# Performance work log

Measured on AMD Instinct MI355X. Metric: run time of the kernel, lower is better.

Reference implementation:

```python
import jax, jax.numpy as jnp
import numpy as np

EPS = 1e-5

def conv1d(x, w, b):
    # x: (N,C,L), w: (O,I,3), stride 1, padding 1 -> same length
    y = jax.lax.conv_general_dilated(x, w, window_strides=(1,), padding=((1, 1),),
                                     dimension_numbers=('NCH', 'OIH', 'NCH'))
    return y + b[None, :, None]

def bn(x, g, b):
    # BatchNorm1d, training-mode batch statistics over (N, L) per channel
    m = x.mean(axis=(0, 2), keepdims=True)
    v = x.var(axis=(0, 2), keepdims=True)
    return (x - m) * jax.lax.rsqrt(v + EPS) * g[None, :, None] + b[None, :, None]

def setup_inputs() -> dict:
    V, E, H, L, NL = 50257, 512, 512, 2048, 2
    D = 1 + NL * 2  # 5 channels in the pre-attention conv stack
    key = jax.random.key(0)
    ks = iter(jax.random.split(key, 48))
    def rn(shape, s=0.02):
        return jax.random.normal(next(ks), shape, dtype=jnp.float32) * s
    inp = dict(
        emb=rn((V, E), 1.0),
        conv1_w=rn((32, D, 3)), conv1_b=rn((32,)),
        conv2_w=rn((D, 32, 3)), conv2_b=rn((D,)),
        conv3_w=rn((1, D, 3)), conv3_b=rn((1,)),
        conv4_w=rn((32, 3, 3)), conv4_b=rn((32,)),
        conv5_w=rn((3, 32, 3)), conv5_b=rn((3,)),
        conv6_w=rn((1, 3, 3)), conv6_b=rn((1,)),
        bn1_g=jnp.ones((32,)), bn1_b=jnp.zeros((32,)),
        bn2_g=jnp.ones((D,)), bn2_b=jnp.zeros((D,)),
        bn3_g=jnp.ones((1,)), bn3_b=jnp.zeros((1,)),
        bn4_g=jnp.ones((32,)), bn4_b=jnp.zeros((32,)),
        bn5_g=jnp.ones((3,)), bn5_b=jnp.zeros((3,)),
        bn6_g=jnp.ones((1,)), bn6_b=jnp.zeros((1,)),
        att_w=rn((L, E)), att_b=rn((L,)),
        gru_wih=rn((4, 3 * H, E)), gru_whh=rn((4, 3 * H, H)),
        gru_bih=rn((4, 3 * H)), gru_bhh=rn((4, 3 * H)),
        lo_w=rn((V, H)), lo_b=rn((V,)),
        h_state=rn((4, 1, H), 1.0),
        encoder_outs=rn((L, 2 * H), 1.0),
        x=jax.random.randint(next(ks), (1,), 0, V),
    )
    return inp

def reference(emb, conv1_w, conv1_b, conv2_w, conv2_b, conv3_w, conv3_b,
              conv4_w, conv4_b, conv5_w, conv5_b, conv6_w, conv6_b,
              bn1_g, bn1_b, bn2_g, bn2_b, bn3_g, bn3_b,
              bn4_g, bn4_b, bn5_g, bn5_b, bn6_g, bn6_b,
              att_w, att_b, gru_wih, gru_whh, gru_bih, gru_bhh,
              lo_w, lo_b, h_state, encoder_outs, x):
    H = h_state.shape[-1]
    # dropout(p=0.1) treated as identity (eval mode / deterministic reference)
    embadded = emb[x].reshape(1, 1, H)                                      # (1,1,512)
    pre = jnp.concatenate([h_state.reshape(1, -1, H), embadded], axis=1)    # (1,5,512)
    c = jax.nn.relu(bn(conv1d(pre, conv1_w, conv1_b), bn1_g, bn1_b))        # (1,32,512)
    pre = jax.nn.relu(bn(conv1d(c, conv2_w, conv2_b) + pre, bn2_g, bn2_b))  # residual, (1,5,512)
    pre = jax.nn.relu(bn(conv1d(pre, conv3_w, conv3_b), bn3_g, bn3_b))      # (1,1,512)
    aw = jax.nn.softmax(pre.reshape(1, -1) @ att_w.T + att_b, axis=1)       # (1,L)
    app = (aw @ encoder_outs).reshape(1, -1, H)                             # (1,2,512) (bidir encoder)
    com = jnp.concatenate([app, embadded], axis=1)                          # (1,3,512)
    c = jax.nn.relu(bn(conv1d(com, conv4_w, conv4_b), bn4_g, bn4_b))        # (1,32,512)
    com = jax.nn.relu(bn(conv1d(c, conv5_w, conv5_b) + com, bn5_g, bn5_b))  # residual, (1,3,512)
    com = jax.nn.relu(bn(conv1d(com, conv6_w, conv6_b), bn6_g, bn6_b))      # (1,1,512)
    # 4-layer stacked GRU, single time step, batch 1 (PyTorch gate order r,z,n)
    xt = com.reshape(H)
    h_new = []
    for l in range(h_state.shape[0]):
        gi = gru_wih[l] @ xt + gru_bih[l]
        gh = gru_whh[l] @ h_state[l, 0] + gru_bhh[l]
        ir, iz, inn = jnp.split(gi, 3)
        hr, hz, hn = jnp.split(gh, 3)
        r = jax.nn.sigmoid(ir + hr)
        z = jax.nn.sigmoid(iz + hz)
        n = jnp.tanh(inn + r * hn)
        xt = (1.0 - z) * n + z * h_state[l, 0]
        h_new.append(xt)
    h_state_new = jnp.stack(h_new)[:, None, :]                              # (4,1,512)
    out = jax.nn.log_softmax((xt @ lo_w.T + lo_b)[None, :], axis=1)         # (1,V)
    return out, h_state_new
```

## Files before the change

### kernel.cpp

```cpp
#include <hip/hip_runtime.h>
#include <hip/hip_bf16.h>

typedef __attribute__((ext_vector_type(4))) float f32x4;

constexpr int WSF_Q     = 0;
constexpr int WSF_ADEN  = 512;
constexpr int WSF_APART = 1024;
constexpr int WSF_XT    = 33792;
constexpr int WSF_LOGV  = 36352;
constexpr int WSF_PM    = 86624;
constexpr int WSF_PS    = 87424;
constexpr int NVOCAB    = 50257;
constexpr int NBLK_V    = 786;

__device__ __forceinline__ float wave_rsum(float v) {
#pragma unroll
    for (int o = 32; o > 0; o >>= 1) v += __shfl_down(v, o);
    return v;
}
__device__ __forceinline__ float sigm(float x) { return 1.0f / (1.0f + __expf(-x)); }

__global__ __launch_bounds__(512) void k_pre(
    const float* __restrict__ emb, const int* __restrict__ xidx,
    const float* __restrict__ hstate,
    const float* __restrict__ w1, const float* __restrict__ b1,
    const float* __restrict__ w2, const float* __restrict__ b2,
    const float* __restrict__ w3, const float* __restrict__ b3,
    const float* __restrict__ g1, const float* __restrict__ bb1,
    const float* __restrict__ g2, const float* __restrict__ bb2,
    const float* __restrict__ g3, const float* __restrict__ bb3,
    float* __restrict__ ws)
{
    constexpr int W1 = 0, B1 = 480, G1 = 512, BB1 = 544;
    constexpr int W2 = 576, B2 = 1056, G2 = 1061, BB2 = 1066;
    constexpr int W3 = 1071, B3 = 1086, G3 = 1087, BB3 = 1088, NW = 1089;
    __shared__ float s_w[NW];
    __shared__ float s_pre[5][512];
    __shared__ float s_y[32][512];
    __shared__ float s_stat[32][2];
    const int tid = threadIdx.x, lane = tid & 63, wid = tid >> 6, l = tid;

    if (tid < 480) s_w[W1 + tid] = w1[tid];
    if (tid < 32) { s_w[B1 + tid] = b1[tid]; s_w[G1 + tid] = g1[tid]; s_w[BB1 + tid] = bb1[tid]; }
    if (tid < 480) s_w[W2 + tid] = w2[tid];
    if (tid < 5) { s_w[B2 + tid] = b2[tid]; s_w[G2 + tid] = g2[tid]; s_w[BB2 + tid] = bb2[tid]; }
    if (tid < 15) s_w[W3 + tid] = w3[tid];
    if (tid == 0) { s_w[B3] = b3[0]; s_w[G3] = g3[0]; s_w[BB3] = bb3[0]; }

    const int x = xidx[0];
#pragma unroll
    for (int c = 0; c < 4; ++c) s_pre[c][l] = hstate[c * 512 + l];
    s_pre[4][l] = emb[(size_t)x * 512 + l];
    __syncthreads();

    float px[5][3];
#pragma unroll
    for (int ic = 0; ic < 5; ++ic) {
        px[ic][0] = (l > 0)   ? s_pre[ic][l-1] : 0.f;
        px[ic][1] =             s_pre[ic][l];
        px[ic][2] = (l < 511) ? s_pre[ic][l+1] : 0.f;
    }
#pragma unroll 4
    for (int oc = 0; oc < 32; ++oc) {
        float a = s_w[B1 + oc];
#pragma unroll
        for (int ic = 0; ic < 5; ++ic)
#pragma unroll
            for (int k = 0; k < 3; ++k)
                a += s_w[W1 + oc*15 + ic*3 + k] * px[ic][k];
        s_y[oc][l] = a;
    }
    __syncthreads();
#pragma unroll
    for (int t = 0; t < 4; ++t) {
        const int oc = wid * 4 + t;
        float s = 0.f, s2 = 0.f;
#pragma unroll
        for (int j = 0; j < 8; ++j) { float v = s_y[oc][lane + j*64]; s += v; s2 += v*v; }
        s = wave_rsum(s); s2 = wave_rsum(s2);
        if (lane == 0) { float m = s/512.f, var = s2/512.f - m*m; s_stat[oc][0] = m; s_stat[oc][1] = rsqrtf(var + 1e-5f); }
    }
    __syncthreads();
#pragma unroll 4
    for (int oc = 0; oc < 32; ++oc)
        s_y[oc][l] = fmaxf((s_y[oc][l] - s_stat[oc][0]) * s_stat[oc][1] * s_w[G1+oc] + s_w[BB1+oc], 0.f);
    __syncthreads();

    float y2[5];
#pragma unroll
    for (int oc = 0; oc < 5; ++oc) y2[oc] = s_w[B2 + oc];
#pragma unroll 2
    for (int ic = 0; ic < 32; ++ic) {
        float c0 = (l > 0)   ? s_y[ic][l-1] : 0.f;
        float c1 =             s_y[ic][l];
        float c2 = (l < 511) ? s_y[ic][l+1] : 0.f;
#pragma unroll
        for (int oc = 0; oc < 5; ++oc) {
            const int base = W2 + (oc*32 + ic)*3;
            y2[oc] += s_w[base]*c0 + s_w[base+1]*c1 + s_w[base+2]*c2;
        }
    }
#pragma unroll
    for (int oc = 0; oc < 5; ++oc) y2[oc] += s_pre[oc][l];
    __syncthreads();
#pragma unroll
    for (int oc = 0; oc < 5; ++oc) s_y[oc][l] = y2[oc];
    __syncthreads();
    if (wid < 5) {
        const int oc = wid;
        float s = 0.f, s2 = 0.f;
#pragma unroll
        for (int j = 0; j < 8; ++j) { float v = s_y[oc][lane + j*64]; s += v; s2 += v*v; }
        s = wave_rsum(s); s2 = wave_rsum(s2);
        if (lane == 0) { float m = s/512.f, var = s2/512.f - m*m; s_stat[oc][0] = m; s_stat[oc][1] = rsqrtf(var + 1e-5f); }
    }
    __syncthreads();
#pragma unroll
    for (int oc = 0; oc < 5; ++oc)
        s_pre[oc][l] = fmaxf((y2[oc] - s_stat[oc][0]) * s_stat[oc][1] * s_w[G2+oc] + s_w[BB2+oc], 0.f);
    __syncthreads();

    float a3 = s_w[B3];
#pragma unroll
    for (int ic = 0; ic < 5; ++ic) {
        float c0 = (l > 0)   ? s_pre[ic][l-1] : 0.f;
        float c1 =             s_pre[ic][l];
        float c2 = (l < 511) ? s_pre[ic][l+1] : 0.f;
        a3 += s_w[W3+ic*3]*c0 + s_w[W3+ic*3+1]*c1 + s_w[W3+ic*3+2]*c2;
    }
    s_y[0][l] = a3;
    __syncthreads();
    if (wid == 0) {
        float s = 0.f, s2 = 0.f;
#pragma unroll
        for (int j = 0; j < 8; ++j) { float v = s_y[0][lane + j*64]; s += v; s2 += v*v; }
        s = wave_rsum(s); s2 = wave_rsum(s2);
        if (lane == 0) { float m = s/512.f, var = s2/512.f - m*m; s_stat[0][0] = m; s_stat[0][1] = rsqrtf(var + 1e-5f); }
    }
    __syncthreads();
    ws[WSF_Q + l] = fmaxf((a3 - s_stat[0][0]) * s_stat[0][1] * s_w[G3] + s_w[BB3], 0.f);
}

__global__ __launch_bounds__(256) void k_att(
    const float* __restrict__ attw, const float* __restrict__ attb,
    const float* __restrict__ enc, float* __restrict__ ws)
{
    __shared__ float s_e[64];
    __shared__ float s_d[4];
    const int tid = threadIdx.x, lane = tid & 63, wid = tid >> 6;
    const int jc = blockIdx.x;

    float q0[4], q1[4];
#pragma unroll
    for (int j = 0; j < 4; ++j) {
        q0[j] = ws[WSF_Q + lane*4 + j];
        q1[j] = ws[WSF_Q + 256 + lane*4 + j];
    }
    float dpart = 0.f;
#pragma unroll 4
    for (int r = 0; r < 16; ++r) {
        const int row = jc * 64 + wid * 16 + r;
        f32x4 w0 = *(const f32x4*)(attw + (size_t)row*512 + lane*4);
        f32x4 w1 = *(const f32x4*)(attw + (size_t)row*512 + 256 + lane*4);
        float a = 0.f;
#pragma unroll
        for (int j = 0; j < 4; ++j) a += w0[j]*q0[j] + w1[j]*q1[j];
        a = wave_rsum(a);
        if (lane == 0) {
            float e = __expf(a + attb[row]);
            s_e[wid*16 + r] = e;
            dpart += e;
        }
    }
    if (lane == 0) s_d[wid] = dpart;
    __syncthreads();
    if (tid == 0) ws[WSF_ADEN + jc] = s_d[0] + s_d[1] + s_d[2] + s_d[3];

    const int col = tid * 4;
    const float* ep = enc + (size_t)(jc * 64) * 1024 + col;
    f32x4 acc = {0.f, 0.f, 0.f, 0.f};
#pragma unroll 8
    for (int jj = 0; jj < 64; ++jj) {
        f32x4 v = *(const f32x4*)(ep + (size_t)jj * 1024);
        acc += s_e[jj] * v;
    }
    *(f32x4*)(ws + WSF_APART + jc * 1024 + col) = acc;
}

__global__ __launch_bounds__(512) void k_post(
    const float* __restrict__ emb, const int* __restrict__ xidx,
    const float* __restrict__ w4, const float* __restrict__ b4,
    const float* __restrict__ w5, const float* __restrict__ b5,
    const float* __restrict__ w6, const float* __restrict__ b6,
    const float* __restrict__ g4, const float* __restrict__ bb4,
    const float* __restrict__ g5, const float* __restrict__ bb5,
    const float* __restrict__ g6, const float* __restrict__ bb6,
    float* __restrict__ ws)
{
    constexpr int W4 = 0, B4 = 288, G4 = 320, BB4 = 352;
    constexpr int W5 = 384, B5 = 672, G5 = 675, BB5 = 678;
    constexpr int W6 = 681, B6 = 690, G6 = 691, BB6 = 692, NW = 693;
    __shared__ float s_w[NW];
    __shared__ float s_com[3][512];
    __shared__ float s_y[32][512];
    __shared__ float s_stat[32][2];
    const int tid = threadIdx.x, lane = tid & 63, wid = tid >> 6, l = tid;

    if (tid < 288) s_w[W4 + tid] = w4[tid];
    if (tid < 32) { s_w[B4 + tid] = b4[tid]; s_w[G4 + tid] = g4[tid]; s_w[BB4 + tid] = bb4[tid]; }
    if (tid < 288) s_w[W5 + tid] = w5[tid];
    if (tid < 3) { s_w[B5 + tid] = b5[tid]; s_w[G5 + tid] = g5[tid]; s_w[BB5 + tid] = bb5[tid]; }
    if (tid < 9) s_w[W6 + tid] = w6[tid];
    if (tid == 0) { s_w[B6] = b6[0]; s_w[G6] = g6[0]; s_w[BB6] = bb6[0]; }

    float den = 0.f;
#pragma unroll 8
    for (int i = 0; i < 32; ++i) den += ws[WSF_ADEN + i];
    const float invS = 1.0f / den;
    float a0 = 0.f, a1 = 0.f;
#pragma unroll 8
    for (int p = 0; p < 32; ++p) {
        a0 += ws[WSF_APART + p*1024 + l];
        a1 += ws[WSF_APART + p*1024 + 512 + l];
    }
    const int x = xidx[0];
    s_com[0][l] = a0 * invS;
    s_com[1][l] = a1 * invS;
    s_com[2][l] = emb[(size_t)x*512 + l];
    __syncthreads();

    float px[3][3];
#pragma unroll
    for (int ic = 0; ic < 3; ++ic) {
        px[ic][0] = (l > 0)   ? s_com[ic][l-1] : 0.f;
        px[ic][1] =             s_com[ic][l];
        px[ic][2] = (l < 511) ? s_com[ic][l+1] : 0.f;
    }
#pragma unroll 4
    for (int oc = 0; oc < 32; ++oc) {
        float a = s_w[B4 + oc];
#pragma unroll
        for (int ic = 0; ic < 3; ++ic)
#pragma unroll
            for (int k = 0; k < 3; ++k)
                a += s_w[W4 + oc*9 + ic*3 + k] * px[ic][k];
        s_y[oc][l] = a;
    }
    __syncthreads();
#pragma unroll
    for (int t = 0; t < 4; ++t) {
        const int oc = wid * 4 + t;
        float s = 0.f, s2 = 0.f;
#pragma unroll
        for (int j = 0; j < 8; ++j) { float v = s_y[oc][lane + j*64]; s += v; s2 += v*v; }
        s = wave_rsum(s); s2 = wave_rsum(s2);
        if (lane == 0) { float m = s/512.f, var = s2/512.f - m*m; s_stat[oc][0] = m; s_stat[oc][1] = rsqrtf(var + 1e-5f); }
    }
    __syncthreads();
#pragma unroll 4
    for (int oc = 0; oc < 32; ++oc)
        s_y[oc][l] = fmaxf((s_y[oc][l] - s_stat[oc][0]) * s_stat[oc][1] * s_w[G4+oc] + s_w[BB4+oc], 0.f);
    __syncthreads();

    float y2[3];
#pragma unroll
    for (int oc = 0; oc < 3; ++oc) y2[oc] = s_w[B5 + oc];
#pragma unroll 2
    for (int ic = 0; ic < 32; ++ic) {
        float c0 = (l > 0)   ? s_y[ic][l-1] : 0.f;
        float c1 =             s_y[ic][l];
        float c2 = (l < 511) ? s_y[ic][l+1] : 0.f;
#pragma unroll
        for (int oc = 0; oc < 3; ++oc) {
            const int base = W5 + (oc*32 + ic)*3;
            y2[oc] += s_w[base]*c0 + s_w[base+1]*c1 + s_w[base+2]*c2;
        }
    }
#pragma unroll
    for (int oc = 0; oc < 3; ++oc) y2[oc] += s_com[oc][l];
    __syncthreads();
#pragma unroll
    for (int oc = 0; oc < 3; ++oc) s_y[oc][l] = y2[oc];
    __syncthreads();
    if (wid < 3) {
        const int oc = wid;
        float s = 0.f, s2 = 0.f;
#pragma unroll
        for (int j = 0; j < 8; ++j) { float v = s_y[oc][lane + j*64]; s += v; s2 += v*v; }
        s = wave_rsum(s); s2 = wave_rsum(s2);
        if (lane == 0) { float m = s/512.f, var = s2/512.f - m*m; s_stat[oc][0] = m; s_stat[oc][1] = rsqrtf(var + 1e-5f); }
    }
    __syncthreads();
#pragma unroll
    for (int oc = 0; oc < 3; ++oc)
        s_com[oc][l] = fmaxf((y2[oc] - s_stat[oc][0]) * s_stat[oc][1] * s_w[G5+oc] + s_w[BB5+oc], 0.f);
    __syncthreads();

    float a6 = s_w[B6];
#pragma unroll
    for (int ic = 0; ic < 3; ++ic) {
        float c0 = (l > 0)   ? s_com[ic][l-1] : 0.f;
        float c1 =             s_com[ic][l];
        float c2 = (l < 511) ? s_com[ic][l+1] : 0.f;
        a6 += s_w[W6+ic*3]*c0 + s_w[W6+ic*3+1]*c1 + s_w[W6+ic*3+2]*c2;
    }
    s_y[0][l] = a6;
    __syncthreads();
    if (wid == 0) {
        float s = 0.f, s2 = 0.f;
#pragma unroll
        for (int j = 0; j < 8; ++j) { float v = s_y[0][lane + j*64]; s += v; s2 += v*v; }
        s = wave_rsum(s); s2 = wave_rsum(s2);
        if (lane == 0) { float m = s/512.f, var = s2/512.f - m*m; s_stat[0][0] = m; s_stat[0][1] = rsqrtf(var + 1e-5f); }
    }
    __syncthreads();
    ws[WSF_XT + l] = fmaxf((a6 - s_stat[0][0]) * s_stat[0][1] * s_w[G6] + s_w[BB6], 0.f);
}

__global__ __launch_bounds__(256) void k_gru(
    const float* __restrict__ wih, const float* __restrict__ whh,
    const float* __restrict__ bih, const float* __restrict__ bhh,
    const float* __restrict__ hstate,
    const float* __restrict__ xt_in, float* __restrict__ xt_out,
    float* __restrict__ hout, int layer)
{
    wih += (size_t)layer * 1536 * 512;
    whh += (size_t)layer * 1536 * 512;
    bih += layer * 1536;
    bhh += layer * 1536;
    const float* hp = hstate + layer * 512;

    const int tid = threadIdx.x, lane = tid & 63, wid = tid >> 6;
    float xq0[4], xq1[4], hq0[4], hq1[4];
#pragma unroll
    for (int j = 0; j < 4; ++j) {
        xq0[j] = xt_in[lane*4 + j];
        xq1[j] = xt_in[256 + lane*4 + j];
        hq0[j] = hp[lane*4 + j];
        hq1[j] = hp[256 + lane*4 + j];
    }
    __shared__ float s_g[8][6];
    const int i0 = blockIdx.x * 8;
#pragma unroll
    for (int t = 0; t < 2; ++t) {
        const int ii = wid * 2 + t;
        const int i = i0 + ii;
        float a[6] = {0.f, 0.f, 0.f, 0.f, 0.f, 0.f};
#pragma unroll
        for (int g = 0; g < 3; ++g) {
            const float* wr = wih + (size_t)(i + g*512) * 512;
            f32x4 w0 = *(const f32x4*)(wr + lane*4);
            f32x4 w1 = *(const f32x4*)(wr + 256 + lane*4);
#pragma unroll
            for (int j = 0; j < 4; ++j) a[g] += w0[j]*xq0[j] + w1[j]*xq1[j];
        }
#pragma unroll
        for (int g = 0; g < 3; ++g) {
            const float* wr = whh + (size_t)(i + g*512) * 512;
            f32x4 w0 = *(const f32x4*)(wr + lane*4);
            f32x4 w1 = *(const f32x4*)(wr + 256 + lane*4);
#pragma unroll
            for (int j = 0; j < 4; ++j) a[3+g] += w0[j]*hq0[j] + w1[j]*hq1[j];
        }
#pragma unroll
        for (int g = 0; g < 6; ++g) a[g] = wave_rsum(a[g]);
        if (lane == 0) {
#pragma unroll
            for (int g = 0; g < 6; ++g) s_g[ii][g] = a[g];
        }
    }
    __syncthreads();
    if (tid < 8) {
        const int i = i0 + tid;
        float ir = s_g[tid][0] + bih[i];
        float iz = s_g[tid][1] + bih[i + 512];
        float in_ = s_g[tid][2] + bih[i + 1024];
        float hr = s_g[tid][3] + bhh[i];
        float hz = s_g[tid][4] + bhh[i + 512];
        float hn = s_g[tid][5] + bhh[i + 1024];
        float r = sigm(ir + hr);
        float z = sigm(iz + hz);
        float n = tanhf(in_ + r * hn);
        float h = (1.f - z) * n + z * hp[i];
        xt_out[i] = h;
        hout[i] = h;
    }
}

__global__ __launch_bounds__(256) void k_vocab(
    const float* __restrict__ low, const float* __restrict__ lob,
    float* __restrict__ ws)
{
    const int tid = threadIdx.x, lane = tid & 63, wid = tid >> 6;
    float q0[4], q1[4];
#pragma unroll
    for (int j = 0; j < 4; ++j) {
        q0[j] = ws[WSF_XT + 4*512 + lane*4 + j];
        q1[j] = ws[WSF_XT + 4*512 + 256 + lane*4 + j];
    }
    const int row0 = blockIdx.x * 64 + wid * 16;
    float m = -INFINITY, s = 0.0f;
#pragma unroll 4
    for (int r = 0; r < 16; ++r) {
        const int row = row0 + r;
        if (row < NVOCAB) {
            f32x4 w0 = *(const f32x4*)(low + (size_t)row*512 + lane*4);
            f32x4 w1 = *(const f32x4*)(low + (size_t)row*512 + 256 + lane*4);
            float a = 0.f;
#pragma unroll
            for (int j = 0; j < 4; ++j) a += w0[j]*q0[j] + w1[j]*q1[j];
            a = wave_rsum(a);
            if (lane == 0) {
                float v = a + lob[row];
                ws[WSF_LOGV + row] = v;
                if (v > m) { s = s * __expf(m - v) + 1.0f; m = v; }
                else       { s += __expf(v - m); }
            }
        }
    }
    __shared__ float smx[4], ssx[4];
    if (lane == 0) { smx[wid] = m; ssx[wid] = s; }
    __syncthreads();
    if (tid == 0) {
        float M = -INFINITY, S = 0.0f;
#pragma unroll
        for (int w = 0; w < 4; ++w) {
            float mb = smx[w], sb = ssx[w];
            if (sb > 0.0f) {
                if (mb > M) { S = S * __expf(M - mb) + sb; M = mb; }
                else        { S += sb * __expf(mb - M); }
            }
        }
        ws[WSF_PM + blockIdx.x] = M;
        ws[WSF_PS + blockIdx.x] = S;
    }
}

__global__ __launch_bounds__(256) void k_outlse(
    const float* __restrict__ ws, float* __restrict__ out)
{
    __shared__ float smx[256], ssx[256];
    const int tid = threadIdx.x;
    float M = -INFINITY, S = 0.0f;
    for (int i = tid; i < NBLK_V; i += 256) {
        float mb = ws[WSF_PM + i], sb = ws[WSF_PS + i];
        if (mb > M) { S = S * __expf(M - mb) + sb; M = mb; }
        else        { S += sb * __expf(mb - M); }
    }
    smx[tid] = M; ssx[tid] = S;
    __syncthreads();
    for (int st = 128; st > 0; st >>= 1) {
        if (tid < st) {
            float mb = smx[tid + st], sb = ssx[tid + st];
            if (sb > 0.0f) {
                if (mb > smx[tid]) { ssx[tid] = ssx[tid] * __expf(smx[tid] - mb) + sb; smx[tid] = mb; }
                else               { ssx[tid] += sb * __expf(mb - smx[tid]); }
            }
        }
        __syncthreads();
    }
    const float lse = smx[0] + logf(ssx[0]);
    const int i = blockIdx.x * 256 + tid;
    if (i < NVOCAB) out[i] = ws[WSF_LOGV + i] - lse;
}

extern "C" void kernel_launch(void* const* d_in, const int* in_sizes, int n_in,
                              void* d_out, int out_size, void* d_ws, size_t ws_size,
                              hipStream_t stream)
{
    (void)in_sizes; (void)n_in; (void)out_size; (void)ws_size;
    const float* emb     = (const float*)d_in[0];
    const float* conv1_w = (const float*)d_in[1];  const float* conv1_b = (const float*)d_in[2];
    const float* conv2_w = (const float*)d_in[3];  const float* conv2_b = (const float*)d_in[4];
    const float* conv3_w = (const float*)d_in[5];  const float* conv3_b = (const float*)d_in[6];
    const float* conv4_w = (const float*)d_in[7];  const float* conv4_b = (const float*)d_in[8];
    const float* conv5_w = (const float*)d_in[9];  const float* conv5_b = (const float*)d_in[10];
    const float* conv6_w = (const float*)d_in[11]; const float* conv6_b = (const float*)d_in[12];
    const float* bn1_g = (const float*)d_in[13];   const float* bn1_b = (const float*)d_in[14];
    const float* bn2_g = (const float*)d_in[15];   const float* bn2_b = (const float*)d_in[16];
    const float* bn3_g = (const float*)d_in[17];   const float* bn3_b = (const float*)d_in[18];
    const float* bn4_g = (const float*)d_in[19];   const float* bn4_b = (const float*)d_in[20];
    const float* bn5_g = (const float*)d_in[21];   const float* bn5_b = (const float*)d_in[22];
    const float* bn6_g = (const float*)d_in[23];   const float* bn6_b = (const float*)d_in[24];
    const float* att_w = (const float*)d_in[25];   const float* att_b = (const float*)d_in[26];
    const float* gru_wih = (const float*)d_in[27]; const float* gru_whh = (const float*)d_in[28];
    const float* gru_bih = (const float*)d_in[29]; const float* gru_bhh = (const float*)d_in[30];
    const float* lo_w = (const float*)d_in[31];    const float* lo_b = (const float*)d_in[32];
    const float* h_state = (const float*)d_in[33];
    const float* enc = (const float*)d_in[34];
    const int* x = (const int*)d_in[35];

    float* ws = (float*)d_ws;
    float* out = (float*)d_out;

    k_pre<<<1, 512, 0, stream>>>(emb, x, h_state,
        conv1_w, conv1_b, conv2_w, conv2_b, conv3_w, conv3_b,
        bn1_g, bn1_b, bn2_g, bn2_b, bn3_g, bn3_b, ws);
    k_att<<<32, 256, 0, stream>>>(att_w, att_b, enc, ws);
    k_post<<<1, 512, 0, stream>>>(emb, x,
        conv4_w, conv4_b, conv5_w, conv5_b, conv6_w, conv6_b,
        bn4_g, bn4_b, bn5_g, bn5_b, bn6_g, bn6_b, ws);
    for (int l = 0; l < 4; ++l) {
        k_gru<<<64, 256, 0, stream>>>(gru_wih, gru_whh, gru_bih, gru_bhh, h_state,
            ws + WSF_XT + l * 512, ws + WSF_XT + (l + 1) * 512,
            out + NVOCAB + l * 512, l);
    }
    k_vocab<<<NBLK_V, 256, 0, stream>>>(lo_w, lo_b, ws);
    k_outlse<<<197, 256, 0, stream>>>(ws, out);
}
```

Baseline: 96.56 us.

## Spread attention and GRU matvecs across more blocks for higher parallelism

```diff
diff --git a/kernel.cpp b/kernel.cpp
--- a/kernel.cpp
+++ b/kernel.cpp
@@ -6,10 +6,10 @@
 constexpr int WSF_Q     = 0;
 constexpr int WSF_ADEN  = 512;
 constexpr int WSF_APART = 1024;
-constexpr int WSF_XT    = 33792;
-constexpr int WSF_LOGV  = 36352;
-constexpr int WSF_PM    = 86624;
-constexpr int WSF_PS    = 87424;
+constexpr int WSF_XT    = 132096;
+constexpr int WSF_LOGV  = 134656;
+constexpr int WSF_PM    = 184960;
+constexpr int WSF_PS    = 185856;
 constexpr int NVOCAB    = 50257;
 constexpr int NBLK_V    = 786;
 
@@ -145,7 +145,7 @@
     const float* __restrict__ attw, const float* __restrict__ attb,
     const float* __restrict__ enc, float* __restrict__ ws)
 {
-    __shared__ float s_e[64];
+    __shared__ float s_e[16];
     __shared__ float s_d[4];
     const int tid = threadIdx.x, lane = tid & 63, wid = tid >> 6;
     const int jc = blockIdx.x;
@@ -157,9 +157,9 @@
         q1[j] = ws[WSF_Q + 256 + lane*4 + j];
     }
     float dpart = 0.f;
-#pragma unroll 4
-    for (int r = 0; r < 16; ++r) {
-        const int row = jc * 64 + wid * 16 + r;
+#pragma unroll
+    for (int r = 0; r < 4; ++r) {
+        const int row = jc * 16 + wid * 4 + r;
         f32x4 w0 = *(const f32x4*)(attw + (size_t)row*512 + lane*4);
         f32x4 w1 = *(const f32x4*)(attw + (size_t)row*512 + 256 + lane*4);
         float a = 0.f;
@@ -168,7 +168,7 @@
         a = wave_rsum(a);
         if (lane == 0) {
             float e = __expf(a + attb[row]);
-            s_e[wid*16 + r] = e;
+            s_e[wid*4 + r] = e;
             dpart += e;
         }
     }
@@ -177,10 +177,10 @@
     if (tid == 0) ws[WSF_ADEN + jc] = s_d[0] + s_d[1] + s_d[2] + s_d[3];
 
     const int col = tid * 4;
-    const float* ep = enc + (size_t)(jc * 64) * 1024 + col;
+    const float* ep = enc + (size_t)(jc * 16) * 1024 + col;
     f32x4 acc = {0.f, 0.f, 0.f, 0.f};
 #pragma unroll 8
-    for (int jj = 0; jj < 64; ++jj) {
+    for (int jj = 0; jj < 16; ++jj) {
         f32x4 v = *(const f32x4*)(ep + (size_t)jj * 1024);
         acc += s_e[jj] * v;
     }
@@ -215,11 +215,11 @@
 
     float den = 0.f;
 #pragma unroll 8
-    for (int i = 0; i < 32; ++i) den += ws[WSF_ADEN + i];
+    for (int i = 0; i < 128; ++i) den += ws[WSF_ADEN + i];
     const float invS = 1.0f / den;
     float a0 = 0.f, a1 = 0.f;
 #pragma unroll 8
-    for (int p = 0; p < 32; ++p) {
+    for (int p = 0; p < 128; ++p) {
         a0 += ws[WSF_APART + p*1024 + l];
         a1 += ws[WSF_APART + p*1024 + 512 + l];
     }
@@ -331,46 +331,33 @@
     const float* hp = hstate + layer * 512;
 
     const int tid = threadIdx.x, lane = tid & 63, wid = tid >> 6;
-    float xq0[4], xq1[4], hq0[4], hq1[4];
+    const int i0 = blockIdx.x * 2;
+    const int lu = wid >> 1;
+    const int useH = wid & 1;
+    const int u = i0 + lu;
+
+    const float* vsrc = useH ? hp : xt_in;
+    const float* wmat = useH ? whh : wih;
+    float v0[4], v1[4];
 #pragma unroll
     for (int j = 0; j < 4; ++j) {
-        xq0[j] = xt_in[lane*4 + j];
-        xq1[j] = xt_in[256 + lane*4 + j];
-        hq0[j] = hp[lane*4 + j];
-        hq1[j] = hp[256 + lane*4 + j];
-    }
-    __shared__ float s_g[8][6];
-    const int i0 = blockIdx.x * 8;
-#pragma unroll
-    for (int t = 0; t < 2; ++t) {
-        const int ii = wid * 2 + t;
-        const int i = i0 + ii;
-        float a[6] = {0.f, 0.f, 0.f, 0.f, 0.f, 0.f};
-#pragma unroll
-        for (int g = 0; g < 3; ++g) {
-            const float* wr = wih + (size_t)(i + g*512) * 512;
-            f32x4 w0 = *(const f32x4*)(wr + lane*4);
-            f32x4 w1 = *(const f32x4*)(wr + 256 + lane*4);
-#pragma unroll
-            for (int j = 0; j < 4; ++j) a[g] += w0[j]*xq0[j] + w1[j]*xq1[j];
-        }
-#pragma unroll
-        for (int g = 0; g < 3; ++g) {
-            const float* wr = whh + (size_t)(i + g*512) * 512;
-            f32x4 w0 = *(const f32x4*)(wr + lane*4);
-            f32x4 w1 = *(const f32x4*)(wr + 256 + lane*4);
-#pragma unroll
-            for (int j = 0; j < 4; ++j) a[3+g] += w0[j]*hq0[j] + w1[j]*hq1[j];
-        }
-#pragma unroll
-        for (int g = 0; g < 6; ++g) a[g] = wave_rsum(a[g]);
-        if (lane == 0) {
-#pragma unroll
-            for (int g = 0; g < 6; ++g) s_g[ii][g] = a[g];
-        }
-    }
-    __syncthreads();
-    if (tid < 8) {
+        v0[j] = vsrc[lane*4 + j];
+        v1[j] = vsrc[256 + lane*4 + j];
+    }
+    __shared__ float s_g[2][6];
+#pragma unroll
+    for (int g = 0; g < 3; ++g) {
+        const float* wr = wmat + (size_t)(u + g*512) * 512;
+        f32x4 w0 = *(const f32x4*)(wr + lane*4);
+        f32x4 w1 = *(const f32x4*)(wr + 256 + lane*4);
+        float a = 0.f;
+#pragma unroll
+        for (int j = 0; j < 4; ++j) a += w0[j]*v0[j] + w1[j]*v1[j];
+        a = wave_rsum(a);
+        if (lane == 0) s_g[lu][useH*3 + g] = a;
+    }
+    __syncthreads();
+    if (tid < 2) {
         const int i = i0 + tid;
         float ir = s_g[tid][0] + bih[i];
         float iz = s_g[tid][1] + bih[i + 512];
@@ -496,12 +483,12 @@
     k_pre<<<1, 512, 0, stream>>>(emb, x, h_state,
         conv1_w, conv1_b, conv2_w, conv2_b, conv3_w, conv3_b,
         bn1_g, bn1_b, bn2_g, bn2_b, bn3_g, bn3_b, ws);
-    k_att<<<32, 256, 0, stream>>>(att_w, att_b, enc, ws);
+    k_att<<<128, 256, 0, stream>>>(att_w, att_b, enc, ws);
     k_post<<<1, 512, 0, stream>>>(emb, x,
         conv4_w, conv4_b, conv5_w, conv5_b, conv6_w, conv6_b,
         bn4_g, bn4_b, bn5_g, bn5_b, bn6_g, bn6_b, ws);
     for (int l = 0; l < 4; ++l) {
-        k_gru<<<64, 256, 0, stream>>>(gru_wih, gru_whh, gru_bih, gru_bhh, h_state,
+        k_gru<<<256, 256, 0, stream>>>(gru_wih, gru_whh, gru_bih, gru_bhh, h_state,
             ws + WSF_XT + l * 512, ws + WSF_XT + (l + 1) * 512,
             out + NVOCAB + l * 512, l);
     }
```

New measurement: 94.81 us. Within noise of the previous version (-1.8%).
